# Performance work log

Measured on AMD Instinct MI355X. Metric: run time of the kernel, lower is better.

## Reference

```python
import jax, jax.numpy as jnp
import numpy as np

H = W = 256
WS = 8      # window size
SS = 4      # shift size
NH = 3      # num heads
EPS = 1e-5


def _rel_pos_index(ws):
    coords = np.stack(np.meshgrid(np.arange(ws), np.arange(ws), indexing='ij')).reshape(2, -1)
    rel = (coords[:, :, None] - coords[:, None, :]).transpose(1, 2, 0)
    rel[..., 0] += ws - 1
    rel[..., 1] += ws - 1
    rel[..., 0] *= 2 * ws - 1
    return rel.sum(-1)  # (ws*ws, ws*ws) int


def _attn_mask(h, w, ws, ss):
    img = np.zeros((h, w))
    cnt = 0
    for hs in (slice(0, -ws), slice(-ws, -ss), slice(-ss, None)):
        for wsl in (slice(0, -ws), slice(-ws, -ss), slice(-ss, None)):
            img[hs, wsl] = cnt
            cnt += 1
    mw = img.reshape(h // ws, ws, w // ws, ws).transpose(0, 2, 1, 3).reshape(-1, ws * ws)
    am = mw[:, None, :] - mw[:, :, None]
    return np.where(am != 0, -100.0, 0.0).astype(np.float32)  # (nW, N, N)


_RPI = jnp.asarray(_rel_pos_index(WS))
_MASK = jnp.asarray(_attn_mask(H, W, WS, SS))


def _ln(x, w, b):
    m = x.mean(-1, keepdims=True)
    v = ((x - m) ** 2).mean(-1, keepdims=True)
    return (x - m) * jax.lax.rsqrt(v + EPS) * w + b


def setup_inputs() -> dict:
    key = jax.random.key(0)
    ks = jax.random.split(key, 6)
    C, DFF = 96, 384
    return {
        'x': jax.random.normal(ks[0], (8, H * W, C), jnp.float32),
        'norm1_w': jnp.ones((C,), jnp.float32),
        'norm1_b': jnp.zeros((C,), jnp.float32),
        'qkv_w': jax.random.normal(ks[1], (3 * C, C), jnp.float32) * 0.02,
        'qkv_b': jnp.zeros((3 * C,), jnp.float32),
        'rpb_table': jax.random.normal(ks[2], ((2 * WS - 1) ** 2, NH), jnp.float32) * 0.02,
        'proj_w': jax.random.normal(ks[3], (C, C), jnp.float32) * 0.02,
        'proj_b': jnp.zeros((C,), jnp.float32),
        'norm2_w': jnp.ones((C,), jnp.float32),
        'norm2_b': jnp.zeros((C,), jnp.float32),
        'mlp_w1': jax.random.normal(ks[4], (DFF, C), jnp.float32) * 0.02,
        'mlp_b1': jnp.zeros((DFF,), jnp.float32),
        'mlp_w2': jax.random.normal(ks[5], (C, DFF), jnp.float32) * 0.02,
        'mlp_b2': jnp.zeros((C,), jnp.float32),
    }


def reference(x, norm1_w, norm1_b, qkv_w, qkv_b, rpb_table, proj_w, proj_b,
              norm2_w, norm2_b, mlp_w1, mlp_b1, mlp_w2, mlp_b2):
    B, L, C = x.shape
    N = WS * WS
    hd = C // NH
    scale = hd ** -0.5

    shortcut = x
    h = _ln(x, norm1_w, norm1_b).reshape(B, H, W, C)
    h = jnp.roll(h, (-SS, -SS), axis=(1, 2))
    # window partition -> (B_ , N, C)
    xw = h.reshape(B, H // WS, WS, W // WS, WS, C).transpose(0, 1, 3, 2, 4, 5).reshape(-1, N, C)
    B_ = xw.shape[0]

    qkv = (xw @ qkv_w.T + qkv_b).reshape(B_, N, 3, NH, hd).transpose(2, 0, 3, 1, 4)
    q, k, v = qkv[0], qkv[1], qkv[2]  # each (B_, NH, N, hd)
    attn = jnp.einsum('bhnd,bhmd->bhnm', q, k) * scale

    bias = rpb_table[_RPI.reshape(-1)].reshape(N, N, NH).transpose(2, 0, 1)  # (NH,N,N)
    attn = attn + bias[None]

    nW = _MASK.shape[0]
    attn = attn.reshape(B_ // nW, nW, NH, N, N) + _MASK[None, :, None]
    attn = jax.nn.softmax(attn.reshape(B_, NH, N, N), axis=-1)

    o = jnp.einsum('bhnm,bhmd->bhnd', attn, v).transpose(0, 2, 1, 3).reshape(B_, N, C)
    o = o @ proj_w.T + proj_b
    # window reverse -> (B, H, W, C)
    o = o.reshape(B, H // WS, W // WS, WS, WS, C).transpose(0, 1, 3, 2, 4, 5).reshape(B, H, W, C)
    o = jnp.roll(o, (SS, SS), axis=(1, 2))

    x1 = shortcut + o.reshape(B, L, C)
    h2 = _ln(x1, norm2_w, norm2_b)
    h2 = jax.nn.gelu(h2 @ mlp_w1.T + mlp_b1, approximate=False) @ mlp_w2.T + mlp_b2
    return x1 + h2
```

## Files before the change

kernel.cpp:

```cpp
#include <hip/hip_runtime.h>
#include <math.h>

#define HH    256
#define WWID  256
#define WSZ   8
#define SSZ   4
#define NHEAD 3
#define CCH   96
#define DFF   384

#define XW_LD 104
#define QK_LD 200
#define VT_LD 72
#define P_LD  72
#define H_LD  200

using bf16x8 = __attribute__((ext_vector_type(8))) short;
using f32x4  = __attribute__((ext_vector_type(4))) float;

#define LOG2E 1.44269504088896f

__device__ __forceinline__ unsigned short f2bf(float f) {
    unsigned u = __float_as_uint(f);
    return (unsigned short)((u + 0x7FFFu + ((u >> 16) & 1u)) >> 16);
}
__device__ __forceinline__ float bf2f(unsigned short s) {
    return __uint_as_float(((unsigned)s) << 16);
}
__device__ __forceinline__ unsigned cvtpk(float lo, float hi) {
    unsigned r;
    asm("v_cvt_pk_bf16_f32 %0, %1, %2" : "=v"(r) : "v"(lo), "v"(hi));
    return r;
}
__device__ __forceinline__ float lo2f(unsigned u) { return __uint_as_float(u << 16); }
__device__ __forceinline__ float hi2f(unsigned u) { return __uint_as_float(u & 0xFFFF0000u); }

__device__ __forceinline__ float gelu_t(float t) {
    float t2 = t * t;
    float u  = t * (0.7978845608028654f + 0.03567740814183f * t2);
    float e  = exp2f(u * 2.885390081777927f);
    float rc = __builtin_amdgcn_rcpf(e + 1.f);
    return t - t * rc;
}

#define WQ_OFF  0
#define WP_OFF  27648
#define W1_OFF  36864
#define W2_OFF  73728
#define CT_OFF  110592

__global__ void __launch_bounds__(256)
prep(const float* __restrict__ qkvw, const float* __restrict__ pw,
     const float* __restrict__ w1, const float* __restrict__ w2,
     const float* __restrict__ rpb, unsigned short* __restrict__ wsq)
{
    int e = blockIdx.x * 256 + threadIdx.x;
    if (e < 110592) {
        const float* W; int Kd, nk, i = e;
        if (i < 27648)      { W = qkvw; Kd = 96;  nk = 3;  }
        else if (i < 36864) { W = pw;   Kd = 96;  nk = 3;  i -= 27648; }
        else if (i < 73728) { W = w1;   Kd = 96;  nk = 3;  i -= 36864; }
        else                { W = w2;   Kd = 384; nk = 12; i -= 73728; }
        int j = i & 7, fe = i >> 3;
        int lane = fe & 63, q = fe >> 6;
        int ks = q % nk, t = q / nk;
        int row = t * 16 + (lane & 15);
        int col = ks * 32 + (lane >> 4) * 8 + j;
        wsq[e] = f2bf(W[(size_t)row * Kd + col]);
    } else if (e < 159744) {
        int i = e - 110592;
        int cls = i / 12288;
        int rem = i - cls * 12288;
        int h = rem >> 12, n = (rem >> 6) & 63, m = rem & 63;
        int rel = ((n >> 3) - (m >> 3) + 7) * 15 + ((n & 7) - (m & 7) + 7);
        float bias = rpb[rel * NHEAD + h];
        int ci = cls >> 1, cj = cls & 1;
        int rn = (ci ? ((n >> 3) < 4 ? 1 : 2) : 0) * 3 + (cj ? ((n & 7) < 4 ? 1 : 2) : 0);
        int rm = (ci ? ((m >> 3) < 4 ? 1 : 2) : 0) * 3 + (cj ? ((m & 7) < 4 ? 1 : 2) : 0);
        float mask = (rn != rm) ? -100.f : 0.f;
        wsq[CT_OFF + i] = f2bf((bias + mask) * LOG2E);
    }
}

__global__ void __launch_bounds__(256, 3)
fused(const float* __restrict__ x,
      const float* __restrict__ n1w, const float* __restrict__ n1b,
      const float* __restrict__ qkvb, const float* __restrict__ pb,
      const float* __restrict__ n2w, const float* __restrict__ n2b,
      const float* __restrict__ b1, const float* __restrict__ b2,
      const unsigned short* __restrict__ wsq,
      float* __restrict__ y)
{
    __shared__ unsigned short SM[24320];
    unsigned short* sR1 = SM;
    unsigned short* sQK = SM + 6912;
    unsigned short* sP  = SM + 19712;

    const int bwin = blockIdx.x;
    const int b  = bwin >> 10;
    const int wi = (bwin >> 5) & 31;
    const int wj = bwin & 31;
    const int tid = threadIdx.x;
    const int lane = tid & 63;
    const int wave = tid >> 6;
    const int l15 = lane & 15;
    const int l16 = lane >> 4;
    const int nb = wave * 16;
    const int sub = lane & 3;

    const int tm  = nb + (lane >> 2);
    const int gh1 = ((wi << 3) + (tm >> 3) + SSZ) & (HH - 1);
    const int gw1 = ((wj << 3) + (tm & 7) + SSZ) & (WWID - 1);
    const size_t rowtm = ((size_t)b * (HH * WWID) + (size_t)gh1 * WWID + gw1) * CCH;

    f32x4 xv[6];
    {
        const float* xr = x + rowtm + sub * 24;
#pragma unroll
        for (int q = 0; q < 6; ++q) xv[q] = *(const f32x4*)(xr + 4 * q);
        float s1 = 0.f, s2 = 0.f;
#pragma unroll
        for (int q = 0; q < 6; ++q)
#pragma unroll
            for (int r = 0; r < 4; ++r) { s1 += xv[q][r]; s2 = fmaf(xv[q][r], xv[q][r], s2); }
        s1 += __shfl_xor(s1, 1);  s2 += __shfl_xor(s2, 1);
        s1 += __shfl_xor(s1, 2);  s2 += __shfl_xor(s2, 2);
        const float mean = s1 * (1.f / CCH);
        const float rstd = rsqrtf(s2 * (1.f / CCH) - mean * mean + 1e-5f);
        unsigned o[12];
#pragma unroll
        for (int q = 0; q < 6; ++q) {
            const f32x4 wv = *(const f32x4*)&n1w[sub * 24 + 4 * q];
            const f32x4 bv = *(const f32x4*)&n1b[sub * 24 + 4 * q];
            float a0 = (xv[q][0] - mean) * rstd * wv[0] + bv[0];
            float a1 = (xv[q][1] - mean) * rstd * wv[1] + bv[1];
            float a2 = (xv[q][2] - mean) * rstd * wv[2] + bv[2];
            float a3 = (xv[q][3] - mean) * rstd * wv[3] + bv[3];
            o[2 * q] = cvtpk(a0, a1); o[2 * q + 1] = cvtpk(a2, a3);
        }
        unsigned* dst = (unsigned*)&sR1[tm * XW_LD + sub * 24];
#pragma unroll
        for (int q = 0; q < 3; ++q) {
            uint4 u; u.x = o[4 * q]; u.y = o[4 * q + 1]; u.z = o[4 * q + 2]; u.w = o[4 * q + 3];
            *(uint4*)(dst + 4 * q) = u;
        }
    }
    __syncthreads();

    bf16x8 afr[4][3];
#pragma unroll
    for (int mt = 0; mt < 4; ++mt)
#pragma unroll
        for (int ks = 0; ks < 3; ++ks)
            afr[mt][ks] = *(const bf16x8*)&sR1[(mt * 16 + l15) * XW_LD + ks * 32 + l16 * 8];
    __syncthreads();

    {
        const float qscale = 0.17677669529663689f * LOG2E;
        for (int nt = wave; nt < 18; nt += 4) {
            f32x4 acc[4] = {{0,0,0,0},{0,0,0,0},{0,0,0,0},{0,0,0,0}};
#pragma unroll
            for (int ks = 0; ks < 3; ++ks) {
                const bf16x8 wf = *(const bf16x8*)(wsq + ((size_t)(nt * 3 + ks) * 64 + lane) * 8);
#pragma unroll
                for (int mt = 0; mt < 4; ++mt)
                    acc[mt] = __builtin_amdgcn_mfma_f32_16x16x32_bf16(wf, afr[mt][ks], acc[mt], 0, 0, 0);
            }
            const f32x4 bias = *(const f32x4*)&qkvb[nt * 16 + 4 * l16];
            if (nt < 6) {
#pragma unroll
                for (int mt = 0; mt < 4; ++mt) {
                    uint2 u;
                    u.x = cvtpk((acc[mt][0] + bias[0]) * qscale, (acc[mt][1] + bias[1]) * qscale);
                    u.y = cvtpk((acc[mt][2] + bias[2]) * qscale, (acc[mt][3] + bias[3]) * qscale);
                    *(uint2*)&sQK[(mt * 16 + l15) * QK_LD + nt * 16 + 4 * l16] = u;
                }
            } else if (nt < 12) {
#pragma unroll
                for (int mt = 0; mt < 4; ++mt) {
                    uint2 u;
                    u.x = cvtpk(acc[mt][0] + bias[0], acc[mt][1] + bias[1]);
                    u.y = cvtpk(acc[mt][2] + bias[2], acc[mt][3] + bias[3]);
                    *(uint2*)&sQK[(mt * 16 + l15) * QK_LD + nt * 16 + 4 * l16] = u;
                }
            } else {
                const int ch = nt * 16 - 192 + 4 * l16;
#pragma unroll
                for (int mt = 0; mt < 4; ++mt) {
                    const unsigned v01 = cvtpk(acc[mt][0] + bias[0], acc[mt][1] + bias[1]);
                    const unsigned v23 = cvtpk(acc[mt][2] + bias[2], acc[mt][3] + bias[3]);
                    sR1[(ch + 0) * VT_LD + mt * 16 + l15] = (unsigned short)v01;
                    sR1[(ch + 1) * VT_LD + mt * 16 + l15] = (unsigned short)(v01 >> 16);
                    sR1[(ch + 2) * VT_LD + mt * 16 + l15] = (unsigned short)v23;
                    sR1[(ch + 3) * VT_LD + mt * 16 + l15] = (unsigned short)(v23 >> 16);
                }
            }
        }
    }
    __syncthreads();

    {
        const int cls = ((wi == 31) ? 2 : 0) + ((wj == 31) ? 1 : 0);
        const unsigned short* ctb = wsq + CT_OFF + cls * 12288;
#pragma unroll 1
        for (int h = 0; h < NHEAD; ++h) {
            const bf16x8 qf = *(const bf16x8*)&sQK[(nb + l15) * QK_LD + h * 32 + l16 * 8];
            f32x4 s[4];
#pragma unroll
            for (int mt = 0; mt < 4; ++mt) {
                const bf16x8 kf = *(const bf16x8*)&sQK[(mt * 16 + l15) * QK_LD + CCH + h * 32 + l16 * 8];
                f32x4 z = {0, 0, 0, 0};
                s[mt] = __builtin_amdgcn_mfma_f32_16x16x32_bf16(kf, qf, z, 0, 0, 0);
            }
            const unsigned short* cth = ctb + h * 4096 + (nb + l15) * 64;
            float p[4][4];
            float rsum = 0.f;
#pragma unroll
            for (int mt = 0; mt < 4; ++mt) {
                const ushort4 c4 = *(const ushort4*)&cth[mt * 16 + 4 * l16];
                const float pv0 = exp2f(s[mt][0] + bf2f(c4.x));
                const float pv1 = exp2f(s[mt][1] + bf2f(c4.y));
                const float pv2 = exp2f(s[mt][2] + bf2f(c4.z));
                const float pv3 = exp2f(s[mt][3] + bf2f(c4.w));
                p[mt][0] = pv0; p[mt][1] = pv1; p[mt][2] = pv2; p[mt][3] = pv3;
                rsum += pv0 + pv1 + pv2 + pv3;
            }
            rsum += __shfl_xor(rsum, 16);
            rsum += __shfl_xor(rsum, 32);
            const float rinv = __builtin_amdgcn_rcpf(rsum);
#pragma unroll
            for (int mt = 0; mt < 4; ++mt) {
                uint2 u;
                u.x = cvtpk(p[mt][0], p[mt][1]);
                u.y = cvtpk(p[mt][2], p[mt][3]);
                *(uint2*)&sP[(nb + l15) * P_LD + mt * 16 + 4 * l16] = u;
            }
            f32x4 o[2] = {{0,0,0,0},{0,0,0,0}};
#pragma unroll
            for (int ks = 0; ks < 2; ++ks) {
                const bf16x8 pf = *(const bf16x8*)&sP[(nb + l15) * P_LD + ks * 32 + l16 * 8];
#pragma unroll
                for (int dt = 0; dt < 2; ++dt) {
                    const bf16x8 vf = *(const bf16x8*)&sR1[(h * 32 + dt * 16 + l15) * VT_LD + ks * 32 + l16 * 8];
                    o[dt] = __builtin_amdgcn_mfma_f32_16x16x32_bf16(vf, pf, o[dt], 0, 0, 0);
                }
            }
#pragma unroll
            for (int dt = 0; dt < 2; ++dt) {
                uint2 u;
                u.x = cvtpk(o[dt][0] * rinv, o[dt][1] * rinv);
                u.y = cvtpk(o[dt][2] * rinv, o[dt][3] * rinv);
                *(uint2*)&sQK[(nb + l15) * QK_LD + h * 32 + dt * 16 + 4 * l16] = u;
            }
        }
    }
    __syncthreads();

    {
        bf16x8 ofr[4][3];
#pragma unroll
        for (int mt = 0; mt < 4; ++mt)
#pragma unroll
            for (int ks = 0; ks < 3; ++ks)
                ofr[mt][ks] = *(const bf16x8*)&sQK[(mt * 16 + l15) * QK_LD + ks * 32 + l16 * 8];
        const unsigned short* wp = wsq + WP_OFF;
        for (int ct = wave; ct < 6; ct += 4) {
            f32x4 acc[4] = {{0,0,0,0},{0,0,0,0},{0,0,0,0},{0,0,0,0}};
#pragma unroll
            for (int ks = 0; ks < 3; ++ks) {
                const bf16x8 wf = *(const bf16x8*)(wp + ((size_t)(ct * 3 + ks) * 64 + lane) * 8);
#pragma unroll
                for (int mt = 0; mt < 4; ++mt)
                    acc[mt] = __builtin_amdgcn_mfma_f32_16x16x32_bf16(wf, ofr[mt][ks], acc[mt], 0, 0, 0);
            }
            const f32x4 pbv = *(const f32x4*)&pb[ct * 16 + 4 * l16];
#pragma unroll
            for (int mt = 0; mt < 4; ++mt) {
                uint2 u;
                u.x = cvtpk(acc[mt][0] + pbv[0], acc[mt][1] + pbv[1]);
                u.y = cvtpk(acc[mt][2] + pbv[2], acc[mt][3] + pbv[3]);
                *(uint2*)&sR1[(mt * 16 + l15) * XW_LD + ct * 16 + 4 * l16] = u;
            }
        }
    }
    __syncthreads();

    float y1tm[6][4];
    {
        const unsigned* src = (const unsigned*)&sR1[tm * XW_LD + sub * 24];
#pragma unroll
        for (int q3 = 0; q3 < 3; ++q3) {
            const uint4 u = *(const uint4*)(src + 4 * q3);
            y1tm[2 * q3][0]     = xv[2 * q3][0] + lo2f(u.x);
            y1tm[2 * q3][1]     = xv[2 * q3][1] + hi2f(u.x);
            y1tm[2 * q3][2]     = xv[2 * q3][2] + lo2f(u.y);
            y1tm[2 * q3][3]     = xv[2 * q3][3] + hi2f(u.y);
            y1tm[2 * q3 + 1][0] = xv[2 * q3 + 1][0] + lo2f(u.z);
            y1tm[2 * q3 + 1][1] = xv[2 * q3 + 1][1] + hi2f(u.z);
            y1tm[2 * q3 + 1][2] = xv[2 * q3 + 1][2] + lo2f(u.w);
            y1tm[2 * q3 + 1][3] = xv[2 * q3 + 1][3] + hi2f(u.w);
        }
        float s1 = 0.f, s2 = 0.f;
#pragma unroll
        for (int q = 0; q < 6; ++q)
#pragma unroll
            for (int r = 0; r < 4; ++r) { s1 += y1tm[q][r]; s2 = fmaf(y1tm[q][r], y1tm[q][r], s2); }
        s1 += __shfl_xor(s1, 1);  s2 += __shfl_xor(s2, 1);
        s1 += __shfl_xor(s1, 2);  s2 += __shfl_xor(s2, 2);
        const float mean = s1 * (1.f / CCH);
        const float rstd = rsqrtf(s2 * (1.f / CCH) - mean * mean + 1e-5f);
        unsigned o[12];
#pragma unroll
        for (int q = 0; q < 6; ++q) {
            const f32x4 wv = *(const f32x4*)&n2w[sub * 24 + 4 * q];
            const f32x4 bv = *(const f32x4*)&n2b[sub * 24 + 4 * q];
            float a0 = (y1tm[q][0] - mean) * rstd * wv[0] + bv[0];
            float a1 = (y1tm[q][1] - mean) * rstd * wv[1] + bv[1];
            float a2 = (y1tm[q][2] - mean) * rstd * wv[2] + bv[2];
            float a3 = (y1tm[q][3] - mean) * rstd * wv[3] + bv[3];
            o[2 * q] = cvtpk(a0, a1); o[2 * q + 1] = cvtpk(a2, a3);
        }
        unsigned* dst = (unsigned*)&sR1[tm * XW_LD + sub * 24];
#pragma unroll
        for (int q = 0; q < 3; ++q) {
            uint4 u; u.x = o[4 * q]; u.y = o[4 * q + 1]; u.z = o[4 * q + 2]; u.w = o[4 * q + 3];
            *(uint4*)(dst + 4 * q) = u;
        }
    }
    __syncthreads();

    bf16x8 xfr[4][3];
#pragma unroll
    for (int mt = 0; mt < 4; ++mt)
#pragma unroll
        for (int ks = 0; ks < 3; ++ks)
            xfr[mt][ks] = *(const bf16x8*)&sR1[(mt * 16 + l15) * XW_LD + ks * 32 + l16 * 8];

    f32x4 acc2[2][4];
#pragma unroll
    for (int ci = 0; ci < 2; ++ci)
#pragma unroll
        for (int mt = 0; mt < 4; ++mt) acc2[ci][mt] = (f32x4){0, 0, 0, 0};
    const unsigned short* w2p = wsq + W2_OFF;
#pragma unroll 1
    for (int half = 0; half < 2; ++half) {
        const unsigned short* w1p = wsq + W1_OFF + (size_t)half * 12 * 3 * 64 * 8;
        for (int nt = wave; nt < 12; nt += 4) {
            f32x4 acc[4] = {{0,0,0,0},{0,0,0,0},{0,0,0,0},{0,0,0,0}};
#pragma unroll
            for (int ks = 0; ks < 3; ++ks) {
                const bf16x8 wf = *(const bf16x8*)(w1p + ((size_t)(nt * 3 + ks) * 64 + lane) * 8);
#pragma unroll
                for (int mt = 0; mt < 4; ++mt)
                    acc[mt] = __builtin_amdgcn_mfma_f32_16x16x32_bf16(wf, xfr[mt][ks], acc[mt], 0, 0, 0);
            }
            const f32x4 b1v = *(const f32x4*)&b1[(half * 12 + nt) * 16 + 4 * l16];
#pragma unroll
            for (int mt = 0; mt < 4; ++mt) {
                uint2 u;
                u.x = cvtpk(gelu_t(acc[mt][0] + b1v[0]), gelu_t(acc[mt][1] + b1v[1]));
                u.y = cvtpk(gelu_t(acc[mt][2] + b1v[2]), gelu_t(acc[mt][3] + b1v[3]));
                *(uint2*)&sQK[(mt * 16 + l15) * H_LD + nt * 16 + 4 * l16] = u;
            }
        }
        __syncthreads();
#pragma unroll
        for (int k6 = 0; k6 < 6; ++k6) {
            bf16x8 hfr[4];
#pragma unroll
            for (int mt = 0; mt < 4; ++mt)
                hfr[mt] = *(const bf16x8*)&sQK[(mt * 16 + l15) * H_LD + k6 * 32 + l16 * 8];
#pragma unroll
            for (int ci = 0; ci < 2; ++ci) {
                const int ct = wave + 4 * ci;
                if (ct < 6) {
                    const bf16x8 wf = *(const bf16x8*)(w2p + ((size_t)(ct * 12 + half * 6 + k6) * 64 + lane) * 8);
#pragma unroll
                    for (int mt = 0; mt < 4; ++mt)
                        acc2[ci][mt] = __builtin_amdgcn_mfma_f32_16x16x32_bf16(wf, hfr[mt], acc2[ci][mt], 0, 0, 0);
                }
            }
        }
        if (half == 0) __syncthreads();
    }

    {
#pragma unroll
        for (int ci = 0; ci < 2; ++ci) {
            const int ct = wave + 4 * ci;
            if (ct < 6) {
                const f32x4 b2v = *(const f32x4*)&b2[ct * 16 + 4 * l16];
#pragma unroll
                for (int mt = 0; mt < 4; ++mt) {
                    uint2 u;
                    u.x = cvtpk(acc2[ci][mt][0] + b2v[0], acc2[ci][mt][1] + b2v[1]);
                    u.y = cvtpk(acc2[ci][mt][2] + b2v[2], acc2[ci][mt][3] + b2v[3]);
                    *(uint2*)&sR1[(mt * 16 + l15) * XW_LD + ct * 16 + 4 * l16] = u;
                }
            }
        }
    }
    __syncthreads();
    {
        const unsigned* src = (const unsigned*)&sR1[tm * XW_LD + sub * 24];
        float* yr = y + rowtm + sub * 24;
#pragma unroll
        for (int q3 = 0; q3 < 3; ++q3) {
            const uint4 u = *(const uint4*)(src + 4 * q3);
            f32x4 o0, o1;
            o0[0] = y1tm[2 * q3][0] + lo2f(u.x);
            o0[1] = y1tm[2 * q3][1] + hi2f(u.x);
            o0[2] = y1tm[2 * q3][2] + lo2f(u.y);
            o0[3] = y1tm[2 * q3][3] + hi2f(u.y);
            o1[0] = y1tm[2 * q3 + 1][0] + lo2f(u.z);
            o1[1] = y1tm[2 * q3 + 1][1] + hi2f(u.z);
            o1[2] = y1tm[2 * q3 + 1][2] + lo2f(u.w);
            o1[3] = y1tm[2 * q3 + 1][3] + hi2f(u.w);
            *(f32x4*)(yr + 8 * q3)     = o0;
            *(f32x4*)(yr + 8 * q3 + 4) = o1;
        }
    }
}

extern "C" void kernel_launch(void* const* d_in, const int* in_sizes, int n_in,
                              void* d_out, int out_size, void* d_ws, size_t ws_size,
                              hipStream_t stream)
{
    const float* x    = (const float*)d_in[0];
    const float* n1w  = (const float*)d_in[1];
    const float* n1b  = (const float*)d_in[2];
    const float* qkvw = (const float*)d_in[3];
    const float* qkvb = (const float*)d_in[4];
    const float* rpb  = (const float*)d_in[5];
    const float* pw   = (const float*)d_in[6];
    const float* pb   = (const float*)d_in[7];
    const float* n2w  = (const float*)d_in[8];
    const float* n2b  = (const float*)d_in[9];
    const float* w1   = (const float*)d_in[10];
    const float* b1   = (const float*)d_in[11];
    const float* w2   = (const float*)d_in[12];
    const float* b2   = (const float*)d_in[13];
    float* out = (float*)d_out;

    unsigned short* wsq = (unsigned short*)d_ws;

    prep<<<dim3(624), dim3(256), 0, stream>>>(qkvw, pw, w1, w2, rpb, wsq);
    fused<<<dim3(8192), dim3(256), 0, stream>>>(x, n1w, n1b, qkvb, pb, n2w, n2b,
                                                b1, b2, wsq, out);
}
```

Measured before the change: 314.9 us.

## Pass softmax probabilities to PV MFMA via lane permutes instead of LDS

Attention probabilities are now rearranged from the QK^T accumulator layout into the PV MFMA operand layout with permlane32_swap and ds_swizzle, instead of a round trip through a shared-memory P buffer. Dropping the P buffer shrinks LDS per block, and the launch bound is raised from 3 to 4 blocks per SIMD group to use that headroom. The aim is to cut LDS traffic and raise occupancy. The risks are register pressure under the tighter launch bound and a wrong lane mapping in the permute sequence.

```diff
diff --git a/kernel.cpp b/kernel.cpp
--- a/kernel.cpp
+++ b/kernel.cpp
@@ -12,11 +12,11 @@
 #define XW_LD 104
 #define QK_LD 200
 #define VT_LD 72
-#define P_LD  72
 #define H_LD  200
 
 using bf16x8 = __attribute__((ext_vector_type(8))) short;
 using f32x4  = __attribute__((ext_vector_type(4))) float;
+using int2v  = __attribute__((ext_vector_type(2))) int;
 
 #define LOG2E 1.44269504088896f
 
@@ -82,7 +82,7 @@
     }
 }
 
-__global__ void __launch_bounds__(256, 3)
+__global__ void __launch_bounds__(256, 4)
 fused(const float* __restrict__ x,
       const float* __restrict__ n1w, const float* __restrict__ n1b,
       const float* __restrict__ qkvb, const float* __restrict__ pb,
@@ -91,10 +91,9 @@
       const unsigned short* __restrict__ wsq,
       float* __restrict__ y)
 {
-    __shared__ unsigned short SM[24320];
+    __shared__ unsigned short SM[19712];
     unsigned short* sR1 = SM;
     unsigned short* sQK = SM + 6912;
-    unsigned short* sP  = SM + 19712;
 
     const int bwin = blockIdx.x;
     const int b  = bwin >> 10;
@@ -202,6 +201,7 @@
     {
         const int cls = ((wi == 31) ? 2 : 0) + ((wj == 31) ? 1 : 0);
         const unsigned short* ctb = wsq + CT_OFF + cls * 12288;
+        const bool godd = (l16 & 1) != 0;
 #pragma unroll 1
         for (int h = 0; h < NHEAD; ++h) {
             const bf16x8 qf = *(const bf16x8*)&sQK[(nb + l15) * QK_LD + h * 32 + l16 * 8];
@@ -213,7 +213,7 @@
                 s[mt] = __builtin_amdgcn_mfma_f32_16x16x32_bf16(kf, qf, z, 0, 0, 0);
             }
             const unsigned short* cth = ctb + h * 4096 + (nb + l15) * 64;
-            float p[4][4];
+            unsigned u[4][2];
             float rsum = 0.f;
 #pragma unroll
             for (int mt = 0; mt < 4; ++mt) {
@@ -222,35 +222,43 @@
                 const float pv1 = exp2f(s[mt][1] + bf2f(c4.y));
                 const float pv2 = exp2f(s[mt][2] + bf2f(c4.z));
                 const float pv3 = exp2f(s[mt][3] + bf2f(c4.w));
-                p[mt][0] = pv0; p[mt][1] = pv1; p[mt][2] = pv2; p[mt][3] = pv3;
                 rsum += pv0 + pv1 + pv2 + pv3;
+                u[mt][0] = cvtpk(pv0, pv1);
+                u[mt][1] = cvtpk(pv2, pv3);
             }
             rsum += __shfl_xor(rsum, 16);
             rsum += __shfl_xor(rsum, 32);
             const float rinv = __builtin_amdgcn_rcpf(rsum);
-#pragma unroll
-            for (int mt = 0; mt < 4; ++mt) {
-                uint2 u;
-                u.x = cvtpk(p[mt][0], p[mt][1]);
-                u.y = cvtpk(p[mt][2], p[mt][3]);
-                *(uint2*)&sP[(nb + l15) * P_LD + mt * 16 + 4 * l16] = u;
-            }
             f32x4 o[2] = {{0,0,0,0},{0,0,0,0}};
 #pragma unroll
             for (int ks = 0; ks < 2; ++ks) {
-                const bf16x8 pf = *(const bf16x8*)&sP[(nb + l15) * P_LD + ks * 32 + l16 * 8];
+                const int2v r0 = __builtin_amdgcn_permlane32_swap(
+                    (int)u[2 * ks][0], (int)u[2 * ks + 1][0], false, false);
+                const int2v r1 = __builtin_amdgcn_permlane32_swap(
+                    (int)u[2 * ks][1], (int)u[2 * ks + 1][1], false, false);
+                const unsigned X0 = (unsigned)r0[0], Y0 = (unsigned)r0[1];
+                const unsigned X1 = (unsigned)r1[0], Y1 = (unsigned)r1[1];
+                const unsigned SX0 = (unsigned)__builtin_amdgcn_ds_swizzle((int)X0, 0x401F);
+                const unsigned SX1 = (unsigned)__builtin_amdgcn_ds_swizzle((int)X1, 0x401F);
+                const unsigned SY0 = (unsigned)__builtin_amdgcn_ds_swizzle((int)Y0, 0x401F);
+                const unsigned SY1 = (unsigned)__builtin_amdgcn_ds_swizzle((int)Y1, 0x401F);
+                union { unsigned w[4]; bf16x8 v; } pk;
+                pk.w[0] = godd ? SY0 : X0;
+                pk.w[1] = godd ? SY1 : X1;
+                pk.w[2] = godd ? Y0 : SX0;
+                pk.w[3] = godd ? Y1 : SX1;
 #pragma unroll
                 for (int dt = 0; dt < 2; ++dt) {
                     const bf16x8 vf = *(const bf16x8*)&sR1[(h * 32 + dt * 16 + l15) * VT_LD + ks * 32 + l16 * 8];
-                    o[dt] = __builtin_amdgcn_mfma_f32_16x16x32_bf16(vf, pf, o[dt], 0, 0, 0);
+                    o[dt] = __builtin_amdgcn_mfma_f32_16x16x32_bf16(vf, pk.v, o[dt], 0, 0, 0);
                 }
             }
 #pragma unroll
             for (int dt = 0; dt < 2; ++dt) {
-                uint2 u;
-                u.x = cvtpk(o[dt][0] * rinv, o[dt][1] * rinv);
-                u.y = cvtpk(o[dt][2] * rinv, o[dt][3] * rinv);
-                *(uint2*)&sQK[(nb + l15) * QK_LD + h * 32 + dt * 16 + 4 * l16] = u;
+                uint2 uo;
+                uo.x = cvtpk(o[dt][0] * rinv, o[dt][1] * rinv);
+                uo.y = cvtpk(o[dt][2] * rinv, o[dt][3] * rinv);
+                *(uint2*)&sQK[(nb + l15) * QK_LD + h * 32 + dt * 16 + 4 * l16] = uo;
             }
         }
     }
```

New measurement: 405.0 us. 1.29x slower.
